# Kernel optimization log

Hardware: AMD Instinct MI355X
Metric: run time of the kernel (lower is better)

The kernel has to match this reference:

```python
import jax, jax.numpy as jnp
import numpy as np

TOL = 0.5          # Time_tolerance
DECAY = 1.0        # decay_rate
RES = 0.03         # integral_resolution
T_MAX = 120.0
G = 4000           # int(T_MAX / RES)


def setup_inputs() -> dict:
    key = jax.random.key(0)
    ks = jax.random.split(key, 8)
    B, N, H = 128, 64, 128
    times0 = jnp.sort(jax.random.uniform(ks[0], (B, N), dtype=jnp.float32) * T_MAX, axis=-1)
    times1 = jnp.sort(jax.random.uniform(ks[1], (B, N), dtype=jnp.float32) * T_MAX, axis=-1)
    states0 = jax.random.randint(ks[2], (B, N), 0, 2, dtype=jnp.int32)
    states1 = jax.random.randint(ks[3], (B, N), 0, 2, dtype=jnp.int32)
    head_times = jnp.sort(jax.random.uniform(ks[4], (B, H), dtype=jnp.float32) * T_MAX, axis=-1)
    head_states = jax.random.randint(ks[5], (B, H), 0, 2, dtype=jnp.int32)
    base = jnp.full((1,), -0.2, dtype=jnp.float32)  # torch.ones(1) * -0.2
    weights = jax.random.normal(ks[6], (2,), dtype=jnp.float32) * 0.1
    return dict(times0=times0, states0=states0, times1=times1, states1=states1,
                head_times=head_times, head_states=head_states, base=base, weights=weights)


def _intensity(t, times0, states0, times1, states1, head_times, head_states, base, wn):
    # t: [B,T] evaluation times; times*: [B,N]; head_*: [B,H]
    te = t[..., None]                                   # [B,T,1]
    t0 = times0[:, None, :]                             # [B,1,N]
    t1 = times1[:, None, :]
    s0 = states0[:, None, :]
    s1 = states1[:, None, :]
    # exp(-decay*(t - tau)); clamp dt>=0 so masked-out (future) events don't overflow
    dec0 = jnp.exp(-DECAY * jnp.maximum(te - t0, 0.0))  # [B,T,N]
    dec1 = jnp.exp(-DECAY * jnp.maximum(te - t1, 0.0))
    # Formula 0: body [0,1], signs [1,1], relations (0 BEFORE 1), (1 BEFORE head)
    A = jnp.where((t0 <= te) & (s0 == 1), dec0, 0.0)                 # history mask + kernel on pred0
    Bm = jnp.where((t1 < te - TOL) & (s1 == 1), dec1, 0.0)           # (t1 BEFORE head) + history mask
    M = (times0[:, :, None] - times1[:, None, :] < -TOL).astype(t.dtype)  # [B,N,N] (t0 BEFORE t1)
    feat0 = jnp.einsum('bti,bij,btj->bt', A, M, Bm)  # sum over itertools.product pairs
    # Formula 1: body [0], sign [0], relation (0 BEFORE head)
    feat1 = jnp.sum(jnp.where((t0 < te - TOL) & (s0 == 0), dec0, 0.0), axis=-1)
    # formula effect: cur_state via idx = sum(t > head_times) - 1 (numpy negative-index wrap)
    cnt = jnp.sum(te > head_times[:, None, :], axis=-1)              # [B,T]
    Hn = head_times.shape[-1]
    cur_state = jnp.take_along_axis(head_states, (cnt - 1) % Hn, axis=-1)
    eff0 = jnp.where(cur_state == 0, 1.0, -1.0).astype(t.dtype)      # head sign 1 -> +1 iff counter_state==1
    eff1 = -eff0                                                      # head sign 0
    return jnp.exp(base[0] + wn[0] * feat0 * eff0 + wn[1] * feat1 * eff1)


def reference(times0, states0, times1, states1, head_times, head_states, base, weights):
    wn = jax.nn.softmax(weights)  # exp(w)/sum exp(w)
    B = times0.shape[0]
    grid = jnp.broadcast_to((jnp.arange(G, dtype=times0.dtype) * RES)[None, :], (B, G))
    lam_grid = _intensity(grid, times0, states0, times1, states1, head_times, head_states, base, wn)
    lam_ev = _intensity(head_times[:, 1:], times0, states0, times1, states1, head_times, head_states, base, wn)
    log_sum = jnp.sum(jnp.log(lam_ev))
    integral = jnp.sum(lam_grid) * RES
    return (log_sum - integral).reshape(1)
```

## Files before the change

### kernel.cpp

```cpp
#include <hip/hip_runtime.h>
#include <math.h>

constexpr int Bb = 128;
constexpr int Nn = 64;
constexpr int Hh = 128;
constexpr int Gg = 4000;
constexpr float  TOLf = 0.5f;
constexpr double RESd = 0.03;

constexpr int GBLK = 8;
constexpr int NGRID = Bb * GBLK;
constexpr int NBLK  = NGRID + Bb;
constexpr int TSTRIDE = 72;

__global__ __launch_bounds__(64) void precompute_kernel(
    const float* __restrict__ times0, const int* __restrict__ states0,
    const float* __restrict__ times1, const int* __restrict__ states1,
    double* __restrict__ Ps_all, double* __restrict__ Qs_all,
    double* __restrict__ SW_all, double* __restrict__ SWP_all,
    int* __restrict__ kT_all)
{
    const int b = blockIdx.x;
    const int i = threadIdx.x;

    __shared__ float  t1s[Nn];
    __shared__ int    j0s[Nn];
    __shared__ double Ps_sh[Nn + 1];

    const float t0 = times0[b * Nn + i];
    const float t1 = times1[b * Nn + i];
    const int   s0 = states0[b * Nn + i];
    const int   s1 = states1[b * Nn + i];
    t1s[i] = t1;
    __syncthreads();

    int j0 = 0;
    #pragma unroll
    for (int j = 0; j < Nn; ++j)
        j0 += (t0 - t1s[j] >= -TOLf) ? 1 : 0;
    j0s[i] = j0;

    const double e0 = exp((double)t0);
    double p = (s1 == 1) ? exp((double)t1) : 0.0;
    double q = (s0 == 0) ? e0 : 0.0;
    double W = (s0 == 1) ? e0 : 0.0;

    double vp = p, vq = q, vw = W;
    #pragma unroll
    for (int off = 1; off < 64; off <<= 1) {
        double op = __shfl_up(vp, off, 64);
        double oq = __shfl_up(vq, off, 64);
        double ow = __shfl_up(vw, off, 64);
        if (i >= off) { vp += op; vq += oq; vw += ow; }
    }
    Ps_sh[i + 1] = vp;
    if (i == 0) Ps_sh[0] = 0.0;
    __syncthreads();

    const double wpj = W * Ps_sh[j0];
    double vwp = wpj;
    #pragma unroll
    for (int off = 1; off < 64; off <<= 1) {
        double o = __shfl_up(vwp, off, 64);
        if (i >= off) vwp += o;
    }

    int kc = 0;
    #pragma unroll
    for (int j = 0; j < Nn; ++j)
        kc += (j0s[j] <= i) ? 1 : 0;

    double* Ps  = Ps_all  + b * TSTRIDE;
    double* Qs  = Qs_all  + b * TSTRIDE;
    double* SW  = SW_all  + b * TSTRIDE;
    double* SWP = SWP_all + b * TSTRIDE;
    int*    kT  = kT_all  + b * TSTRIDE;

    Ps[i + 1]  = vp;  Qs[i + 1]  = vq;
    SW[i + 1]  = vw;  SWP[i + 1] = vwp;
    kT[i] = kc;
    if (i == 0) {
        Ps[0] = 0.0; Qs[0] = 0.0; SW[0] = 0.0; SWP[0] = 0.0;
        kT[Nn] = Nn;
    }
}

__global__ __launch_bounds__(256) void eval_kernel(
    const float* __restrict__ times0, const float* __restrict__ times1,
    const float* __restrict__ head_times, const int* __restrict__ head_states,
    const float* __restrict__ base, const float* __restrict__ weights,
    const double* __restrict__ Ps_all, const double* __restrict__ Qs_all,
    const double* __restrict__ SW_all, const double* __restrict__ SWP_all,
    const int* __restrict__ kT_all,
    double* __restrict__ partials)
{
    __shared__ float  t0s[Nn], t1s[Nn];
    __shared__ float  hts[Hh];
    __shared__ int    hss[Hh];
    __shared__ double Ps[Nn + 1], Qs[Nn + 1], SW[Nn + 1], SWP[Nn + 1];
    __shared__ int    kT[Nn + 1];
    __shared__ double redsh[4];

    const int tid = threadIdx.x;
    const bool isEvent = blockIdx.x >= (unsigned)NGRID;
    const int b = isEvent ? (blockIdx.x - NGRID) : (blockIdx.x / GBLK);

    if (tid < Nn) {
        t0s[tid] = times0[b * Nn + tid];
        t1s[tid] = times1[b * Nn + tid];
    } else if (tid >= 64 && tid < 64 + Nn + 1) {
        const int k = tid - 64;
        Ps[k]  = Ps_all [b * TSTRIDE + k];
        Qs[k]  = Qs_all [b * TSTRIDE + k];
        SW[k]  = SW_all [b * TSTRIDE + k];
        SWP[k] = SWP_all[b * TSTRIDE + k];
        kT[k]  = kT_all [b * TSTRIDE + k];
    }
    if (tid >= 128) {
        const int k = tid - 128;
        hts[k] = head_times[b * Hh + k];
        hss[k] = head_states[b * Hh + k];
    }
    __syncthreads();

    const double w0 = (double)weights[0], w1 = (double)weights[1];
    const double mw = fmax(w0, w1);
    const double ew0 = exp(w0 - mw), ew1 = exp(w1 - mw);
    const double wn0 = ew0 / (ew0 + ew1), wn1 = ew1 / (ew0 + ew1);
    const double bse = (double)base[0];

    auto evalPoint = [&](float t, bool ev) -> double {
        const float thr = t - TOLf;
        int lo = 0, hi = Nn;
        while (lo < hi) { int m = (lo + hi) >> 1; if (t1s[m] < thr) lo = m + 1; else hi = m; }
        const int c = lo;
        lo = 0; hi = Nn;
        while (lo < hi) { int m = (lo + hi) >> 1; if (t0s[m] < thr) lo = m + 1; else hi = m; }
        const int c0 = lo;
        lo = 0; hi = Nn;
        while (lo < hi) { int m = (lo + hi) >> 1; if (t0s[m] <= t) lo = m + 1; else hi = m; }
        const int c1 = lo;
        lo = 0; hi = Hh;
        while (lo < hi) { int m = (lo + hi) >> 1; if (hts[m] < t) lo = m + 1; else hi = m; }
        const int cnt = lo;

        const int m = min(c1, kT[c]);
        const double Pc = Ps[c];
        const double a = Pc * SW[m] - SWP[m];
        const double ed = exp(-(double)t);
        const double feat0 = a * ed * ed;
        const double feat1 = Qs[c0] * ed;

        const int cur = hss[((unsigned)(cnt - 1)) & (unsigned)(Hh - 1)];
        const double eff0 = (cur == 0) ? 1.0 : -1.0;
        const double loglam = bse + (wn0 * feat0 - wn1 * feat1) * eff0;
        return ev ? loglam : (-RESd * exp(loglam));
    };

    double contrib = 0.0;
    if (isEvent) {
        if (tid >= 1 && tid < Hh) contrib = evalPoint(hts[tid], true);
    } else {
        const int gbase = (blockIdx.x % GBLK) * 512;
        const int g0 = gbase + tid, g1 = gbase + tid + 256;
        if (g0 < Gg) contrib  = evalPoint((float)g0 * 0.03f, false);
        if (g1 < Gg) contrib += evalPoint((float)g1 * 0.03f, false);
    }

    double v = contrib;
    #pragma unroll
    for (int off = 32; off > 0; off >>= 1) v += __shfl_down(v, off, 64);
    if ((tid & 63) == 0) redsh[tid >> 6] = v;
    __syncthreads();
    if (tid == 0) partials[blockIdx.x] = redsh[0] + redsh[1] + redsh[2] + redsh[3];
}

__global__ __launch_bounds__(256) void finalize_kernel(
    const double* __restrict__ partials, float* __restrict__ out)
{
    __shared__ double redsh[4];
    const int tid = threadIdx.x;
    double v = 0.0;
    for (int i = tid; i < NBLK; i += 256) v += partials[i];
    #pragma unroll
    for (int off = 32; off > 0; off >>= 1) v += __shfl_down(v, off, 64);
    if ((tid & 63) == 0) redsh[tid >> 6] = v;
    __syncthreads();
    if (tid == 0) out[0] = (float)(redsh[0] + redsh[1] + redsh[2] + redsh[3]);
}

extern "C" void kernel_launch(void* const* d_in, const int* in_sizes, int n_in,
                              void* d_out, int out_size, void* d_ws, size_t ws_size,
                              hipStream_t stream) {
    const float* times0      = (const float*)d_in[0];
    const int*   states0     = (const int*)  d_in[1];
    const float* times1      = (const float*)d_in[2];
    const int*   states1     = (const int*)  d_in[3];
    const float* head_times  = (const float*)d_in[4];
    const int*   head_states = (const int*)  d_in[5];
    const float* base        = (const float*)d_in[6];
    const float* weights     = (const float*)d_in[7];

    double* Ps_all  = (double*)d_ws;
    double* Qs_all  = Ps_all  + Bb * TSTRIDE;
    double* SW_all  = Qs_all  + Bb * TSTRIDE;
    double* SWP_all = SW_all  + Bb * TSTRIDE;
    int*    kT_all  = (int*)(SWP_all + Bb * TSTRIDE);
    double* partials = (double*)(kT_all + Bb * TSTRIDE);

    precompute_kernel<<<Bb, 64, 0, stream>>>(times0, states0, times1, states1,
                                             Ps_all, Qs_all, SW_all, SWP_all, kT_all);
    eval_kernel<<<NBLK, 256, 0, stream>>>(times0, times1, head_times, head_states,
                                          base, weights,
                                          Ps_all, Qs_all, SW_all, SWP_all, kT_all,
                                          partials);
    finalize_kernel<<<1, 256, 0, stream>>>(partials, (float*)d_out);
}
```

Measured before the change: 80.99 us.

## Rebase grid exponentials per block, use branchless searches and float fast-exp

Grid points are spread over twice as many blocks, with one point per thread instead of two. Each block pre-scales its prefix-sum tables by exp(-tbase), so the per-point decay becomes a small-range float __expf instead of a double exp. The while-loop binary searches become unrolled branchless lower and upper bound searches. The softmax weights are computed once per block into shared memory. In exchange, more per-point arithmetic runs in float, which could reduce accuracy, and the table load layout is reorganised across threads.

```diff
diff --git a/kernel.cpp b/kernel.cpp
--- a/kernel.cpp
+++ b/kernel.cpp
@@ -8,10 +8,42 @@
 constexpr float  TOLf = 0.5f;
 constexpr double RESd = 0.03;
 
-constexpr int GBLK = 8;
+constexpr int GBLK  = 16;
 constexpr int NGRID = Bb * GBLK;
 constexpr int NBLK  = NGRID + Bb;
 constexpr int TSTRIDE = 72;
+
+__device__ __forceinline__ int lb64(const float* __restrict__ a, float key) {
+    int lo = (a[31] < key) ? 32 : 0;
+    lo += (a[lo + 15] < key) ? 16 : 0;
+    lo += (a[lo + 7]  < key) ? 8  : 0;
+    lo += (a[lo + 3]  < key) ? 4  : 0;
+    lo += (a[lo + 1]  < key) ? 2  : 0;
+    lo += (a[lo]      < key) ? 1  : 0;
+    lo += (a[lo]      < key) ? 1  : 0;
+    return lo;
+}
+__device__ __forceinline__ int ub64(const float* __restrict__ a, float key) {
+    int lo = (a[31] <= key) ? 32 : 0;
+    lo += (a[lo + 15] <= key) ? 16 : 0;
+    lo += (a[lo + 7]  <= key) ? 8  : 0;
+    lo += (a[lo + 3]  <= key) ? 4  : 0;
+    lo += (a[lo + 1]  <= key) ? 2  : 0;
+    lo += (a[lo]      <= key) ? 1  : 0;
+    lo += (a[lo]      <= key) ? 1  : 0;
+    return lo;
+}
+__device__ __forceinline__ int lb128(const float* __restrict__ a, float key) {
+    int lo = (a[63] < key) ? 64 : 0;
+    lo += (a[lo + 31] < key) ? 32 : 0;
+    lo += (a[lo + 15] < key) ? 16 : 0;
+    lo += (a[lo + 7]  < key) ? 8  : 0;
+    lo += (a[lo + 3]  < key) ? 4  : 0;
+    lo += (a[lo + 1]  < key) ? 2  : 0;
+    lo += (a[lo]      < key) ? 1  : 0;
+    lo += (a[lo]      < key) ? 1  : 0;
+    return lo;
+}
 
 __global__ __launch_bounds__(64) void precompute_kernel(
     const float* __restrict__ times0, const int* __restrict__ states0,
@@ -41,11 +73,11 @@
     j0s[i] = j0;
 
     const double e0 = exp((double)t0);
-    double p = (s1 == 1) ? exp((double)t1) : 0.0;
-    double q = (s0 == 0) ? e0 : 0.0;
-    double W = (s0 == 1) ? e0 : 0.0;
-
-    double vp = p, vq = q, vw = W;
+    double vp = (s1 == 1) ? exp((double)t1) : 0.0;
+    double vq = (s0 == 0) ? e0 : 0.0;
+    const double W = (s0 == 1) ? e0 : 0.0;
+    double vw = W;
+
     #pragma unroll
     for (int off = 1; off < 64; off <<= 1) {
         double op = __shfl_up(vp, off, 64);
@@ -57,8 +89,7 @@
     if (i == 0) Ps_sh[0] = 0.0;
     __syncthreads();
 
-    const double wpj = W * Ps_sh[j0];
-    double vwp = wpj;
+    double vwp = W * Ps_sh[j0];
     #pragma unroll
     for (int off = 1; off < 64; off <<= 1) {
         double o = __shfl_up(vwp, off, 64);
@@ -99,72 +130,90 @@
     __shared__ int    hss[Hh];
     __shared__ double Ps[Nn + 1], Qs[Nn + 1], SW[Nn + 1], SWP[Nn + 1];
     __shared__ int    kT[Nn + 1];
+    __shared__ double wsh[3];
     __shared__ double redsh[4];
 
     const int tid = threadIdx.x;
     const bool isEvent = blockIdx.x >= (unsigned)NGRID;
-    const int b = isEvent ? (blockIdx.x - NGRID) : (blockIdx.x / GBLK);
+    const int b     = isEvent ? (blockIdx.x - NGRID) : (blockIdx.x >> 4);
+    const int gbase = isEvent ? 0 : ((blockIdx.x & 15) << 8);
+    const double tbase = (double)gbase * 0.03;
 
     if (tid < Nn) {
         t0s[tid] = times0[b * Nn + tid];
         t1s[tid] = times1[b * Nn + tid];
-    } else if (tid >= 64 && tid < 64 + Nn + 1) {
+    } else if (tid < 192) {
         const int k = tid - 64;
-        Ps[k]  = Ps_all [b * TSTRIDE + k];
-        Qs[k]  = Qs_all [b * TSTRIDE + k];
-        SW[k]  = SW_all [b * TSTRIDE + k];
-        SWP[k] = SWP_all[b * TSTRIDE + k];
-        kT[k]  = kT_all [b * TSTRIDE + k];
-    }
-    if (tid >= 128) {
-        const int k = tid - 128;
         hts[k] = head_times[b * Hh + k];
         hss[k] = head_states[b * Hh + k];
-    }
-    __syncthreads();
-
-    const double w0 = (double)weights[0], w1 = (double)weights[1];
-    const double mw = fmax(w0, w1);
-    const double ew0 = exp(w0 - mw), ew1 = exp(w1 - mw);
-    const double wn0 = ew0 / (ew0 + ew1), wn1 = ew1 / (ew0 + ew1);
-    const double bse = (double)base[0];
-
-    auto evalPoint = [&](float t, bool ev) -> double {
-        const float thr = t - TOLf;
-        int lo = 0, hi = Nn;
-        while (lo < hi) { int m = (lo + hi) >> 1; if (t1s[m] < thr) lo = m + 1; else hi = m; }
-        const int c = lo;
-        lo = 0; hi = Nn;
-        while (lo < hi) { int m = (lo + hi) >> 1; if (t0s[m] < thr) lo = m + 1; else hi = m; }
-        const int c0 = lo;
-        lo = 0; hi = Nn;
-        while (lo < hi) { int m = (lo + hi) >> 1; if (t0s[m] <= t) lo = m + 1; else hi = m; }
-        const int c1 = lo;
-        lo = 0; hi = Hh;
-        while (lo < hi) { int m = (lo + hi) >> 1; if (hts[m] < t) lo = m + 1; else hi = m; }
-        const int cnt = lo;
-
-        const int m = min(c1, kT[c]);
-        const double Pc = Ps[c];
-        const double a = Pc * SW[m] - SWP[m];
-        const double ed = exp(-(double)t);
-        const double feat0 = a * ed * ed;
-        const double feat1 = Qs[c0] * ed;
-
-        const int cur = hss[((unsigned)(cnt - 1)) & (unsigned)(Hh - 1)];
-        const double eff0 = (cur == 0) ? 1.0 : -1.0;
-        const double loglam = bse + (wn0 * feat0 - wn1 * feat1) * eff0;
-        return ev ? loglam : (-RESd * exp(loglam));
-    };
+    } else {
+        const double sE = isEvent ? 1.0 : exp(-tbase);
+        int k = tid - 192;
+        const int base_i = b * TSTRIDE;
+        Ps[k]  = Ps_all [base_i + k] * sE;
+        Qs[k]  = Qs_all [base_i + k] * sE;
+        SW[k]  = SW_all [base_i + k] * sE;
+        SWP[k] = SWP_all[base_i + k] * (sE * sE);
+        kT[k]  = kT_all [base_i + k];
+        if (tid == 192) {
+            k = Nn;
+            Ps[k]  = Ps_all [base_i + k] * sE;
+            Qs[k]  = Qs_all [base_i + k] * sE;
+            SW[k]  = SW_all [base_i + k] * sE;
+            SWP[k] = SWP_all[base_i + k] * (sE * sE);
+            kT[k]  = kT_all [base_i + k];
+        }
+    }
+    if (tid == 0) {
+        const double w0 = (double)weights[0], w1 = (double)weights[1];
+        const double mw = fmax(w0, w1);
+        const double e0 = exp(w0 - mw), e1 = exp(w1 - mw);
+        wsh[0] = e0 / (e0 + e1);
+        wsh[1] = e1 / (e0 + e1);
+        wsh[2] = (double)base[0];
+    }
+    __syncthreads();
 
     double contrib = 0.0;
+
     if (isEvent) {
-        if (tid >= 1 && tid < Hh) contrib = evalPoint(hts[tid], true);
+        if (tid >= 1 && tid < Hh) {
+            const float tf = hts[tid];
+            const float thr = tf - TOLf;
+            const int c   = lb64(t1s, thr);
+            const int c0  = lb64(t0s, thr);
+            const int c1  = ub64(t0s, tf);
+            const int cnt = lb128(hts, tf);
+
+            const int m = min(c1, kT[c]);
+            const double a  = Ps[c] * SW[m] - SWP[m];
+            const double ed = exp(-(double)tf);
+            const double f0 = a * ed * ed;
+            const double f1 = Qs[c0] * ed;
+            const int cur = hss[((unsigned)(cnt - 1)) & (unsigned)(Hh - 1)];
+            const double eff = (cur == 0) ? 1.0 : -1.0;
+            contrib = wsh[2] + eff * (wsh[0] * f0 - wsh[1] * f1);
+        }
     } else {
-        const int gbase = (blockIdx.x % GBLK) * 512;
-        const int g0 = gbase + tid, g1 = gbase + tid + 256;
-        if (g0 < Gg) contrib  = evalPoint((float)g0 * 0.03f, false);
-        if (g1 < Gg) contrib += evalPoint((float)g1 * 0.03f, false);
+        const int g = gbase + tid;
+        if (g < Gg) {
+            const float tf = (float)g * 0.03f;
+            const float thr = tf - TOLf;
+            const int c   = lb64(t1s, thr);
+            const int c0  = lb64(t0s, thr);
+            const int c1  = ub64(t0s, tf);
+            const int cnt = lb128(hts, tf);
+
+            const int m = min(c1, kT[c]);
+            const double a = Ps[c] * SW[m] - SWP[m];
+            const double dt = (double)tf - tbase;
+            const float f0 = (float)a * __expf((float)(-2.0 * dt));
+            const float f1 = (float)Qs[c0] * __expf((float)(-dt));
+            const int cur = hss[((unsigned)(cnt - 1)) & (unsigned)(Hh - 1)];
+            const float eff = (cur == 0) ? 1.0f : -1.0f;
+            const float ll = (float)wsh[2] + eff * ((float)wsh[0] * f0 - (float)wsh[1] * f1);
+            contrib = -RESd * (double)__expf(ll);
+        }
     }
 
     double v = contrib;
```

Measured after the change: 77.64 us. -4.1%, faster.
